# Kernel optimization log

Hardware: AMD Instinct MI355X
Metric: run time of the kernel (lower is better)

Reference implementation:

```python
import jax, jax.numpy as jnp
import numpy as np

EPS = 1e-12  # F.normalize default eps


def setup_inputs() -> dict:
    key = jax.random.key(0)
    ks = jax.random.split(key, 8)
    B, T, D, S = 512, 256, 256, 8
    inputs = jax.random.normal(ks[0], (B, T, D), dtype=jnp.float32)
    lengths = jax.random.randint(ks[1], (B,), 1, T + 1, dtype=jnp.int32)
    keys = jax.random.uniform(ks[2], (S, D), minval=-0.1, maxval=0.1, dtype=jnp.float32)
    xav = 1.0 / np.sqrt(D)  # xavier_normal std for square matrix
    U = jax.random.normal(ks[3], (D, D), dtype=jnp.float32) * xav
    V = jax.random.normal(ks[4], (D, D), dtype=jnp.float32) * xav
    W = jax.random.normal(ks[5], (D, D), dtype=jnp.float32) * xav
    gate_bias = jnp.zeros((1,), dtype=jnp.float32)
    state_bias = jnp.zeros((1, D), dtype=jnp.float32)
    return {"inputs": inputs, "lengths": lengths, "keys": keys, "U": U,
            "V": V, "W": W, "gate_bias": gate_bias, "state_bias": state_bias}


def reference(inputs, lengths, keys, U, V, W, gate_bias, state_bias):
    # inputs: [B, T, D]; keys: [S, D]; states carried as [B, S, D]
    B, T, D = inputs.shape
    S = keys.shape[0]
    keyV = keys @ V  # [S, D], loop-invariant
    init_states = jnp.broadcast_to(keys[None], (B, S, D))  # zero_state
    mask = (jnp.arange(T)[:, None] < lengths[None, :])  # [T, B]

    def step(states, xm):
        x, m = xm  # x: [B, D], m: [B]
        # gate: <x, state_j> + <x, key_j> + bias  -> [B, S]
        g = jax.nn.sigmoid(jnp.einsum('bd,bsd->bs', x, states)
                           + x @ keys.T + gate_bias)
        # candidate: state@U + key@V + x@W + state_bias -> [B, S, D]
        h_tilda = jax.nn.elu(jnp.einsum('bsd,de->bse', states, U)
                             + keyV[None]
                             + (x @ W)[:, None, :]
                             + state_bias[None])
        h = states + g[..., None] * h_tilda
        h = h / jnp.maximum(jnp.linalg.norm(h, axis=-1, keepdims=True), EPS)
        new_states = jnp.where(m[:, None, None], h, states)
        return new_states, None

    final_states, _ = jax.lax.scan(step, init_states,
                                   (jnp.swapaxes(inputs, 0, 1), mask))
    return final_states  # [B, S, D] == torch.stack(hiddens, dim=1)
```

## Files before the change

### kernel.cpp

```cpp
#include <hip/hip_runtime.h>
#include <math.h>

namespace {
constexpr int kB = 512;
constexpr int kT = 256;
constexpr int kD = 256;
constexpr int kS = 8;
constexpr int kStRow = 292;
constexpr int kRedRow = 20;

__device__ __forceinline__ int physk(int k) { return k + ((k >> 5) << 2); }

template <int CTRL>
__device__ __forceinline__ float dpp_add(float v) {
  int p = __builtin_amdgcn_update_dpp(0, __float_as_int(v), CTRL, 0xF, 0xF, false);
  return v + __int_as_float(p);
}
}

__global__ __launch_bounds__(256, 2)
void xw_gemm_kernel(const float* __restrict__ X, const float* __restrict__ W,
                    const int* __restrict__ lengths, float* __restrict__ XW) {
  const int m0 = blockIdx.x * 32;
  const int b = m0 >> 8;
  const int t0 = m0 & 255;
  if (t0 >= lengths[b]) return;

  __shared__ float Xs[32][kD];
  const int tid = threadIdx.x;
  const int j  = tid & 63;
  const int rg = tid >> 6;

  const float4* Xg4 = (const float4*)(X + (size_t)m0 * kD);
  float4* Xs4 = (float4*)&Xs[0][0];
  for (int i = tid; i < 32 * kD / 4; i += 256) Xs4[i] = Xg4[i];
  __syncthreads();

  float4 acc[8];
#pragma unroll
  for (int i = 0; i < 8; ++i) acc[i] = make_float4(0.f, 0.f, 0.f, 0.f);

  const float4* W4 = (const float4*)W;
  const float4* Xrow = (const float4*)&Xs[rg * 8][0];

  for (int k4 = 0; k4 < kD / 4; ++k4) {
    float4 w0 = W4[(size_t)(4 * k4 + 0) * 64 + j];
    float4 w1 = W4[(size_t)(4 * k4 + 1) * 64 + j];
    float4 w2 = W4[(size_t)(4 * k4 + 2) * 64 + j];
    float4 w3 = W4[(size_t)(4 * k4 + 3) * 64 + j];
#pragma unroll
    for (int i = 0; i < 8; ++i) {
      float4 x = Xrow[i * 64 + k4];
      acc[i].x = fmaf(x.x, w0.x, fmaf(x.y, w1.x, fmaf(x.z, w2.x, fmaf(x.w, w3.x, acc[i].x))));
      acc[i].y = fmaf(x.x, w0.y, fmaf(x.y, w1.y, fmaf(x.z, w2.y, fmaf(x.w, w3.y, acc[i].y))));
      acc[i].z = fmaf(x.x, w0.z, fmaf(x.y, w1.z, fmaf(x.z, w2.z, fmaf(x.w, w3.z, acc[i].z))));
      acc[i].w = fmaf(x.x, w0.w, fmaf(x.y, w1.w, fmaf(x.z, w2.w, fmaf(x.w, w3.w, acc[i].w))));
    }
  }
  float4* XW4 = (float4*)XW;
#pragma unroll
  for (int i = 0; i < 8; ++i)
    XW4[(size_t)(m0 + rg * 8 + i) * 64 + j] = acc[i];
}

__global__ __launch_bounds__(256, 4)
void gk_kernel(const float* __restrict__ inputs, const float* __restrict__ keys,
               const int* __restrict__ lengths, float* __restrict__ GK) {
  const int b = blockIdx.x;
  const int tid = threadIdx.x;
  const int lane = tid & 63;
  const int wid = tid >> 6;
  const int len = lengths[b];

  __shared__ float4 Ks4[kS * 64];
  for (int i = tid; i < kS * 64; i += 256) Ks4[i] = ((const float4*)keys)[i];
  __syncthreads();

  const float4* X4 = (const float4*)inputs;
  for (int t = wid; t < len; t += 4) {
    float4 x = X4[((size_t)b * kT + t) * 64 + lane];
    float p[kS];
#pragma unroll
    for (int s = 0; s < kS; ++s) {
      float4 kk = Ks4[s * 64 + lane];
      p[s] = fmaf(x.x, kk.x, fmaf(x.y, kk.y, fmaf(x.z, kk.z, x.w * kk.w)));
    }
#pragma unroll
    for (int off = 32; off >= 1; off >>= 1) {
#pragma unroll
      for (int s = 0; s < kS; ++s) p[s] += __shfl_xor(p[s], off, 64);
    }
    if (lane == 0) {
      float* g = GK + ((size_t)b * kT + t) * kS;
#pragma unroll
      for (int s = 0; s < kS; ++s) g[s] = p[s];
    }
  }
}

__global__ __launch_bounds__(512)
void sort_lengths_kernel(const int* __restrict__ lengths, int* __restrict__ order) {
  __shared__ int L[kB];
  const int i = threadIdx.x;
  L[i] = lengths[i];
  __syncthreads();
  const int li = L[i];
  int r = 0;
  for (int j = 0; j < kB; ++j) {
    const int lj = L[j];
    r += (lj > li || (lj == li && j < i)) ? 1 : 0;
  }
  order[r] = i;
}

__global__ __launch_bounds__(1024, 4)
void dynmem_rec7_kernel(const float* __restrict__ inputs,
                        const int*   __restrict__ lengths,
                        const float* __restrict__ keys,
                        const float* __restrict__ U,
                        const float* __restrict__ V,
                        const float* __restrict__ gate_bias,
                        const float* __restrict__ state_bias,
                        const float* __restrict__ XW,
                        const float* __restrict__ GK,
                        const int*   __restrict__ order,
                        float* __restrict__ out)
{
  const int blk = blockIdx.x;
  const int bA = order[blk];
  const int bB = order[kB - 1 - blk];
  const int tid = threadIdx.x;
  const int w = tid >> 6;
  const int lane = tid & 63;
  const int q = lane & 7;
  const int jj = lane >> 3;
  const int p = w * 8 + jj;
  const int c0 = 2 * p;
  const int c0p = physk(c0);
  const int hoff = lane & 8;

  __shared__ float StA[kS * kStRow];
  __shared__ float StB[kS * kStRow];
  __shared__ float KVL[kS * kD];
  __shared__ float redGA[kS * kRedRow], redGB[kS * kRedRow];
  __shared__ float redNA[kS * kRedRow], redNB[kS * kRedRow];

  for (int i = tid; i < kS * kD; i += 1024) {
    int s = i >> 8, dd = i & 255;
    float kv = keys[i];
    int pa = s * kStRow + physk(dd);
    StA[pa] = kv;
    StB[pa] = kv;
  }

  float2 u2[32];
#pragma unroll
  for (int kk = 0; kk < 32; ++kk)
    u2[kk] = *(const float2*)(U + (size_t)(q * 32 + kk) * kD + c0);

  {
    const int h4 = tid >> 8, d = tid & 255;
    float a0 = 0.f, a1 = 0.f;
    const float* Vc = V + d;
    const float* K0 = keys + (size_t)h4 * kD;
    const float* K1 = keys + (size_t)(h4 + 4) * kD;
    for (int k = 0; k < kD; ++k) {
      float v = Vc[(size_t)k * kD];
      a0 = fmaf(K0[k], v, a0);
      a1 = fmaf(K1[k], v, a1);
    }
    float sb = state_bias[d];
    KVL[h4 * kD + d] = a0 + sb;
    KVL[(h4 + 4) * kD + d] = a1 + sb;
  }

  const float gb = gate_bias[0];
  int lenA = lengths[bA]; lenA = lenA < 0 ? 0 : (lenA > kT ? kT : lenA);
  int lenB = lengths[bB]; lenB = lenB < 0 ? 0 : (lenB > kT ? kT : lenB);

  __syncthreads();

  const float2 kvq = *(const float2*)(KVL + q * kD + c0);
  float2 srA = *(const float2*)(StA + q * kStRow + c0p);
  float2 srB = *(const float2*)(StB + q * kStRow + c0p);

  const float* SA = StA + q * 36;
  const float* SB = StB + q * 36;

  for (int t = 0; t < lenA; ++t) {
    const bool dB = t < lenB;
    const size_t baseA = ((size_t)bA * kT + t) * (size_t)kD;
    const size_t baseB = ((size_t)bB * kT + t) * (size_t)kD;

    const float2 xwA = *(const float2*)(XW + baseA + c0);
    const float gkA = GK[((size_t)bA * kT + t) * kS + q];

    {
      float2 xA = *(const float2*)(inputs + baseA + c0);
      float pg = fmaf(xA.x, srA.x, xA.y * srA.y);
      pg += __shfl_xor(pg, 8, 64);
      pg += __shfl_xor(pg, 16, 64);
      pg += __shfl_xor(pg, 32, 64);
      if (lane < 8) redGA[lane * kRedRow + w] = pg;
    }
    if (dB) {
      float2 xB = *(const float2*)(inputs + baseB + c0);
      float pg = fmaf(xB.x, srB.x, xB.y * srB.y);
      pg += __shfl_xor(pg, 8, 64);
      pg += __shfl_xor(pg, 16, 64);
      pg += __shfl_xor(pg, 32, 64);
      if (lane < 8) redGB[lane * kRedRow + w] = pg;
    }

    float caA, cbA, caB = 0.f, cbB = 0.f;
    {
      float C0[8], C1[8];
#pragma unroll
      for (int s = 0; s < 8; ++s) { C0[s] = 0.f; C1[s] = 0.f; }
#pragma unroll
      for (int k4 = 0; k4 < 8; ++k4) {
#pragma unroll
        for (int s = 0; s < 8; ++s) {
          float4 sv = *(const float4*)(SA + s * kStRow + 4 * k4);
          C0[s] = fmaf(sv.x, u2[4 * k4 + 0].x, C0[s]);
          C0[s] = fmaf(sv.y, u2[4 * k4 + 1].x, C0[s]);
          C0[s] = fmaf(sv.z, u2[4 * k4 + 2].x, C0[s]);
          C0[s] = fmaf(sv.w, u2[4 * k4 + 3].x, C0[s]);
          C1[s] = fmaf(sv.x, u2[4 * k4 + 0].y, C1[s]);
          C1[s] = fmaf(sv.y, u2[4 * k4 + 1].y, C1[s]);
          C1[s] = fmaf(sv.z, u2[4 * k4 + 2].y, C1[s]);
          C1[s] = fmaf(sv.w, u2[4 * k4 + 3].y, C1[s]);
        }
      }
#pragma unroll
      for (int s = 0; s < 8; ++s) {
        C0[s] = dpp_add<0xB1>(C0[s]);  C1[s] = dpp_add<0xB1>(C1[s]);
        C0[s] = dpp_add<0x4E>(C0[s]);  C1[s] = dpp_add<0x4E>(C1[s]);
        C0[s] = dpp_add<0x141>(C0[s]); C1[s] = dpp_add<0x141>(C1[s]);
      }
      caA = C0[0]; cbA = C1[0];
#pragma unroll
      for (int s = 1; s < 8; ++s) {
        if (q == s) { caA = C0[s]; cbA = C1[s]; }
      }
    }

    float2 xwB = make_float2(0.f, 0.f);
    float gkB = 0.f;
    if (dB) {
      xwB = *(const float2*)(XW + baseB + c0);
      gkB = GK[((size_t)bB * kT + t) * kS + q];
    }

    if (dB) {
      float C0[8], C1[8];
#pragma unroll
      for (int s = 0; s < 8; ++s) { C0[s] = 0.f; C1[s] = 0.f; }
#pragma unroll
      for (int k4 = 0; k4 < 8; ++k4) {
#pragma unroll
        for (int s = 0; s < 8; ++s) {
          float4 sv = *(const float4*)(SB + s * kStRow + 4 * k4);
          C0[s] = fmaf(sv.x, u2[4 * k4 + 0].x, C0[s]);
          C0[s] = fmaf(sv.y, u2[4 * k4 + 1].x, C0[s]);
          C0[s] = fmaf(sv.z, u2[4 * k4 + 2].x, C0[s]);
          C0[s] = fmaf(sv.w, u2[4 * k4 + 3].x, C0[s]);
          C1[s] = fmaf(sv.x, u2[4 * k4 + 0].y, C1[s]);
          C1[s] = fmaf(sv.y, u2[4 * k4 + 1].y, C1[s]);
          C1[s] = fmaf(sv.z, u2[4 * k4 + 2].y, C1[s]);
          C1[s] = fmaf(sv.w, u2[4 * k4 + 3].y, C1[s]);
        }
      }
#pragma unroll
      for (int s = 0; s < 8; ++s) {
        C0[s] = dpp_add<0xB1>(C0[s]);  C1[s] = dpp_add<0xB1>(C1[s]);
        C0[s] = dpp_add<0x4E>(C0[s]);  C1[s] = dpp_add<0x4E>(C1[s]);
        C0[s] = dpp_add<0x141>(C0[s]); C1[s] = dpp_add<0x141>(C1[s]);
      }
      caB = C0[0]; cbB = C1[0];
#pragma unroll
      for (int s = 1; s < 8; ++s) {
        if (q == s) { caB = C0[s]; cbB = C1[s]; }
      }
    }

    __syncthreads();

    float2 hA = make_float2(0.f, 0.f), hB = make_float2(0.f, 0.f);
    {
      const float* rg = redGA + q * kRedRow + hoff;
      float4 ra = *(const float4*)(rg);
      float4 rb = *(const float4*)(rg + 4);
      float gh = ((ra.x + ra.y) + (ra.z + ra.w)) + ((rb.x + rb.y) + (rb.z + rb.w));
      float gs = gh + __shfl_xor(gh, 8, 64) + gkA + gb;
      float g = 1.f / (1.f + expf(-gs));
      float t0 = caA + kvq.x + xwA.x; t0 = t0 > 0.f ? t0 : expm1f(t0);
      float t1 = cbA + kvq.y + xwA.y; t1 = t1 > 0.f ? t1 : expm1f(t1);
      hA.x = fmaf(g, t0, srA.x);
      hA.y = fmaf(g, t1, srA.y);
      float pn = fmaf(hA.x, hA.x, hA.y * hA.y);
      pn += __shfl_xor(pn, 8, 64);
      pn += __shfl_xor(pn, 16, 64);
      pn += __shfl_xor(pn, 32, 64);
      if (lane < 8) redNA[lane * kRedRow + w] = pn;
    }
    if (dB) {
      const float* rg = redGB + q * kRedRow + hoff;
      float4 ra = *(const float4*)(rg);
      float4 rb = *(const float4*)(rg + 4);
      float gh = ((ra.x + ra.y) + (ra.z + ra.w)) + ((rb.x + rb.y) + (rb.z + rb.w));
      float gs = gh + __shfl_xor(gh, 8, 64) + gkB + gb;
      float g = 1.f / (1.f + expf(-gs));
      float t0 = caB + kvq.x + xwB.x; t0 = t0 > 0.f ? t0 : expm1f(t0);
      float t1 = cbB + kvq.y + xwB.y; t1 = t1 > 0.f ? t1 : expm1f(t1);
      hB.x = fmaf(g, t0, srB.x);
      hB.y = fmaf(g, t1, srB.y);
      float pn = fmaf(hB.x, hB.x, hB.y * hB.y);
      pn += __shfl_xor(pn, 8, 64);
      pn += __shfl_xor(pn, 16, 64);
      pn += __shfl_xor(pn, 32, 64);
      if (lane < 8) redNB[lane * kRedRow + w] = pn;
    }
    __syncthreads();

    {
      const float* rn = redNA + q * kRedRow + hoff;
      float4 na = *(const float4*)(rn);
      float4 nb = *(const float4*)(rn + 4);
      float nh = ((na.x + na.y) + (na.z + na.w)) + ((nb.x + nb.y) + (nb.z + nb.w));
      float ns = nh + __shfl_xor(nh, 8, 64);
      float inh = 1.f / fmaxf(sqrtf(ns), 1e-12f);
      srA.x = hA.x * inh;
      srA.y = hA.y * inh;
      *(float2*)(StA + q * kStRow + c0p) = srA;
    }
    if (dB) {
      const float* rn = redNB + q * kRedRow + hoff;
      float4 na = *(const float4*)(rn);
      float4 nb = *(const float4*)(rn + 4);
      float nh = ((na.x + na.y) + (na.z + na.w)) + ((nb.x + nb.y) + (nb.z + nb.w));
      float ns = nh + __shfl_xor(nh, 8, 64);
      float inh = 1.f / fmaxf(sqrtf(ns), 1e-12f);
      srB.x = hB.x * inh;
      srB.y = hB.y * inh;
      *(float2*)(StB + q * kStRow + c0p) = srB;
    }
    __syncthreads();
  }

  for (int i = tid; i < kS * kD; i += 1024) {
    int s = i >> 8, dd = i & 255;
    int pa = s * kStRow + physk(dd);
    out[(size_t)bA * kS * kD + i] = StA[pa];
    out[(size_t)bB * kS * kD + i] = StB[pa];
  }
}

extern "C" void kernel_launch(void* const* d_in, const int* in_sizes, int n_in,
                              void* d_out, int out_size, void* d_ws, size_t ws_size,
                              hipStream_t stream) {
  const float* inputs     = (const float*)d_in[0];
  const int*   lengths    = (const int*)  d_in[1];
  const float* keys       = (const float*)d_in[2];
  const float* U          = (const float*)d_in[3];
  const float* V          = (const float*)d_in[4];
  const float* W          = (const float*)d_in[5];
  const float* gate_bias  = (const float*)d_in[6];
  const float* state_bias = (const float*)d_in[7];

  const size_t xw_elems = (size_t)kB * kT * kD;
  const size_t gk_elems = (size_t)kB * kT * kS;
  float* XW = (float*)d_ws;
  float* GK = (float*)d_ws + xw_elems;
  int*   order = (int*)((float*)d_ws + xw_elems + gk_elems);

  sort_lengths_kernel<<<dim3(1), dim3(512), 0, stream>>>(lengths, order);
  xw_gemm_kernel<<<dim3((kB * kT) / 32), dim3(256), 0, stream>>>(inputs, W, lengths, XW);
  gk_kernel<<<dim3(kB), dim3(256), 0, stream>>>(inputs, keys, lengths, GK);
  dynmem_rec7_kernel<<<dim3(kB / 2), dim3(1024), 0, stream>>>(
      inputs, lengths, keys, U, V, gate_bias, state_bias, XW, GK, order, (float*)d_out);
}
```

Baseline: 2.369 ms.

## Defer normalization into next step to drop one barrier per timestep

The recurrence now stores the unnormalized state in shared memory and applies the inverse norm lazily at the start of the next step. Because the matvec and gate dot product are linear, they are scaled by the inverse norm afterwards. This removes the third __syncthreads and the separate normalize/store phase from each timestep. It also swaps expf/expm1f for __expf and moves the XW/GK loads later in the step. The norm buffers are initialized so the first step sees a unit scale, and a final pass normalizes the output. This trades slight precision differences (fast exp, expm1 replaced by exp-1) for shorter per-step latency.

Result: slower. 2.998 ms (+26.5%).

```diff
diff --git a/kernel.cpp b/kernel.cpp
--- a/kernel.cpp
+++ b/kernel.cpp
@@ -114,7 +114,7 @@
 }
 
 __global__ __launch_bounds__(1024, 4)
-void dynmem_rec7_kernel(const float* __restrict__ inputs,
+void dynmem_rec8_kernel(const float* __restrict__ inputs,
                         const int*   __restrict__ lengths,
                         const float* __restrict__ keys,
                         const float* __restrict__ U,
@@ -144,6 +144,7 @@
   __shared__ float KVL[kS * kD];
   __shared__ float redGA[kS * kRedRow], redGB[kS * kRedRow];
   __shared__ float redNA[kS * kRedRow], redNB[kS * kRedRow];
+  __shared__ float inhFA[kS], inhFB[kS];
 
   for (int i = tid; i < kS * kD; i += 1024) {
     int s = i >> 8, dd = i & 255;
@@ -151,6 +152,11 @@
     int pa = s * kStRow + physk(dd);
     StA[pa] = kv;
     StB[pa] = kv;
+  }
+  for (int i = tid; i < kS * 16; i += 1024) {
+    int s = i >> 4, ww = i & 15;
+    redNA[s * kRedRow + ww] = 0.0625f;
+    redNB[s * kRedRow + ww] = 0.0625f;
   }
 
   float2 u2[32];
@@ -181,23 +187,41 @@
   __syncthreads();
 
   const float2 kvq = *(const float2*)(KVL + q * kD + c0);
-  float2 srA = *(const float2*)(StA + q * kStRow + c0p);
-  float2 srB = *(const float2*)(StB + q * kStRow + c0p);
-
   const float* SA = StA + q * 36;
   const float* SB = StB + q * 36;
+  float* stpA = StA + q * kStRow + c0p;
+  float* stpB = StB + q * kStRow + c0p;
 
   for (int t = 0; t < lenA; ++t) {
     const bool dB = t < lenB;
     const size_t baseA = ((size_t)bA * kT + t) * (size_t)kD;
     const size_t baseB = ((size_t)bB * kT + t) * (size_t)kD;
 
-    const float2 xwA = *(const float2*)(XW + baseA + c0);
-    const float gkA = GK[((size_t)bA * kT + t) * kS + q];
+    float inhA, inhB = 1.f;
+    {
+      const float* rn = redNA + q * kRedRow + hoff;
+      float4 na = *(const float4*)(rn);
+      float4 nb = *(const float4*)(rn + 4);
+      float nh = ((na.x + na.y) + (na.z + na.w)) + ((nb.x + nb.y) + (nb.z + nb.w));
+      float ns = nh + __shfl_xor(nh, 8, 64);
+      inhA = 1.f / fmaxf(sqrtf(ns), 1e-12f);
+    }
+    if (dB) {
+      const float* rn = redNB + q * kRedRow + hoff;
+      float4 na = *(const float4*)(rn);
+      float4 nb = *(const float4*)(rn + 4);
+      float nh = ((na.x + na.y) + (na.z + na.w)) + ((nb.x + nb.y) + (nb.z + nb.w));
+      float ns = nh + __shfl_xor(nh, 8, 64);
+      inhB = 1.f / fmaxf(sqrtf(ns), 1e-12f);
+    }
+
+    const float2 stA2 = *(const float2*)stpA;
+    float2 stB2 = make_float2(0.f, 0.f);
+    if (dB) stB2 = *(const float2*)stpB;
 
     {
       float2 xA = *(const float2*)(inputs + baseA + c0);
-      float pg = fmaf(xA.x, srA.x, xA.y * srA.y);
+      float pg = fmaf(xA.x, stA2.x, xA.y * stA2.y);
       pg += __shfl_xor(pg, 8, 64);
       pg += __shfl_xor(pg, 16, 64);
       pg += __shfl_xor(pg, 32, 64);
@@ -205,7 +229,7 @@
     }
     if (dB) {
       float2 xB = *(const float2*)(inputs + baseB + c0);
-      float pg = fmaf(xB.x, srB.x, xB.y * srB.y);
+      float pg = fmaf(xB.x, stB2.x, xB.y * stB2.y);
       pg += __shfl_xor(pg, 8, 64);
       pg += __shfl_xor(pg, 16, 64);
       pg += __shfl_xor(pg, 32, 64);
@@ -244,14 +268,6 @@
         if (q == s) { caA = C0[s]; cbA = C1[s]; }
       }
     }
-
-    float2 xwB = make_float2(0.f, 0.f);
-    float gkB = 0.f;
-    if (dB) {
-      xwB = *(const float2*)(XW + baseB + c0);
-      gkB = GK[((size_t)bB * kT + t) * kS + q];
-    }
-
     if (dB) {
       float C0[8], C1[8];
 #pragma unroll
@@ -284,75 +300,75 @@
       }
     }
 
+    const float2 xwA = *(const float2*)(XW + baseA + c0);
+    const float gkA = GK[((size_t)bA * kT + t) * kS + q];
+    float2 xwB = make_float2(0.f, 0.f);
+    float gkB = 0.f;
+    if (dB) {
+      xwB = *(const float2*)(XW + baseB + c0);
+      gkB = GK[((size_t)bB * kT + t) * kS + q];
+    }
+
     __syncthreads();
 
-    float2 hA = make_float2(0.f, 0.f), hB = make_float2(0.f, 0.f);
     {
       const float* rg = redGA + q * kRedRow + hoff;
       float4 ra = *(const float4*)(rg);
       float4 rb = *(const float4*)(rg + 4);
       float gh = ((ra.x + ra.y) + (ra.z + ra.w)) + ((rb.x + rb.y) + (rb.z + rb.w));
-      float gs = gh + __shfl_xor(gh, 8, 64) + gkA + gb;
-      float g = 1.f / (1.f + expf(-gs));
-      float t0 = caA + kvq.x + xwA.x; t0 = t0 > 0.f ? t0 : expm1f(t0);
-      float t1 = cbA + kvq.y + xwA.y; t1 = t1 > 0.f ? t1 : expm1f(t1);
-      hA.x = fmaf(g, t0, srA.x);
-      hA.y = fmaf(g, t1, srA.y);
-      float pn = fmaf(hA.x, hA.x, hA.y * hA.y);
+      gh += __shfl_xor(gh, 8, 64);
+      float gs = fmaf(gh, inhA, gkA + gb);
+      float g = 1.f / (1.f + __expf(-gs));
+      float t0 = fmaf(caA, inhA, kvq.x) + xwA.x; t0 = t0 > 0.f ? t0 : (__expf(t0) - 1.f);
+      float t1 = fmaf(cbA, inhA, kvq.y) + xwA.y; t1 = t1 > 0.f ? t1 : (__expf(t1) - 1.f);
+      float h0 = fmaf(g, t0, stA2.x * inhA);
+      float h1 = fmaf(g, t1, stA2.y * inhA);
+      float pn = fmaf(h0, h0, h1 * h1);
       pn += __shfl_xor(pn, 8, 64);
       pn += __shfl_xor(pn, 16, 64);
       pn += __shfl_xor(pn, 32, 64);
       if (lane < 8) redNA[lane * kRedRow + w] = pn;
+      *(float2*)stpA = make_float2(h0, h1);
     }
     if (dB) {
       const float* rg = redGB + q * kRedRow + hoff;
       float4 ra = *(const float4*)(rg);
       float4 rb = *(const float4*)(rg + 4);
       float gh = ((ra.x + ra.y) + (ra.z + ra.w)) + ((rb.x + rb.y) + (rb.z + rb.w));
-      float gs = gh + __shfl_xor(gh, 8, 64) + gkB + gb;
-      float g = 1.f / (1.f + expf(-gs));
-      float t0 = caB + kvq.x + xwB.x; t0 = t0 > 0.f ? t0 : expm1f(t0);
-      float t1 = cbB + kvq.y + xwB.y; t1 = t1 > 0.f ? t1 : expm1f(t1);
-      hB.x = fmaf(g, t0, srB.x);
-      hB.y = fmaf(g, t1, srB.y);
-      float pn = fmaf(hB.x, hB.x, hB.y * hB.y);
+      gh += __shfl_xor(gh, 8, 64);
+      float gs = fmaf(gh, inhB, gkB + gb);
+      float g = 1.f / (1.f + __expf(-gs));
+      float t0 = fmaf(caB, inhB, kvq.x) + xwB.x; t0 = t0 > 0.f ? t0 : (__expf(t0) - 1.f);
+      float t1 = fmaf(cbB, inhB, kvq.y) + xwB.y; t1 = t1 > 0.f ? t1 : (__expf(t1) - 1.f);
+      float h0 = fmaf(g, t0, stB2.x * inhB);
+      float h1 = fmaf(g, t1, stB2.y * inhB);
+      float pn = fmaf(h0, h0, h1 * h1);
       pn += __shfl_xor(pn, 8, 64);
       pn += __shfl_xor(pn, 16, 64);
       pn += __shfl_xor(pn, 32, 64);
       if (lane < 8) redNB[lane * kRedRow + w] = pn;
+      *(float2*)stpB = make_float2(h0, h1);
     }
     __syncthreads();
-
-    {
-      const float* rn = redNA + q * kRedRow + hoff;
-      float4 na = *(const float4*)(rn);
-      float4 nb = *(const float4*)(rn + 4);
-      float nh = ((na.x + na.y) + (na.z + na.w)) + ((nb.x + nb.y) + (nb.z + nb.w));
-      float ns = nh + __shfl_xor(nh, 8, 64);
-      float inh = 1.f / fmaxf(sqrtf(ns), 1e-12f);
-      srA.x = hA.x * inh;
-      srA.y = hA.y * inh;
-      *(float2*)(StA + q * kStRow + c0p) = srA;
-    }
-    if (dB) {
-      const float* rn = redNB + q * kRedRow + hoff;
-      float4 na = *(const float4*)(rn);
-      float4 nb = *(const float4*)(rn + 4);
-      float nh = ((na.x + na.y) + (na.z + na.w)) + ((nb.x + nb.y) + (nb.z + nb.w));
-      float ns = nh + __shfl_xor(nh, 8, 64);
-      float inh = 1.f / fmaxf(sqrtf(ns), 1e-12f);
-      srB.x = hB.x * inh;
-      srB.y = hB.y * inh;
-      *(float2*)(StB + q * kStRow + c0p) = srB;
-    }
-    __syncthreads();
-  }
+  }
+
+  if (tid < 8) {
+    float s = 0.f;
+    for (int ww = 0; ww < 16; ++ww) s += redNA[tid * kRedRow + ww];
+    inhFA[tid] = 1.f / fmaxf(sqrtf(s), 1e-12f);
+  } else if (tid < 16) {
+    const int s8 = tid - 8;
+    float s = 0.f;
+    for (int ww = 0; ww < 16; ++ww) s += redNB[s8 * kRedRow + ww];
+    inhFB[s8] = 1.f / fmaxf(sqrtf(s), 1e-12f);
+  }
+  __syncthreads();
 
   for (int i = tid; i < kS * kD; i += 1024) {
     int s = i >> 8, dd = i & 255;
     int pa = s * kStRow + physk(dd);
-    out[(size_t)bA * kS * kD + i] = StA[pa];
-    out[(size_t)bB * kS * kD + i] = StB[pa];
+    out[(size_t)bA * kS * kD + i] = StA[pa] * inhFA[s];
+    out[(size_t)bB * kS * kD + i] = StB[pa] * inhFB[s];
   }
 }
 
@@ -377,6 +393,6 @@
   sort_lengths_kernel<<<dim3(1), dim3(512), 0, stream>>>(lengths, order);
   xw_gemm_kernel<<<dim3((kB * kT) / 32), dim3(256), 0, stream>>>(inputs, W, lengths, XW);
   gk_kernel<<<dim3(kB), dim3(256), 0, stream>>>(inputs, keys, lengths, GK);
-  dynmem_rec7_kernel<<<dim3(kB / 2), dim3(1024), 0, stream>>>(
+  dynmem_rec8_kernel<<<dim3(kB / 2), dim3(1024), 0, stream>>>(
       inputs, lengths, keys, U, V, gate_bias, state_bias, XW, GK, order, (float*)d_out);
 }
```
